# Performance work log

Hardware: AMD Instinct MI355X
Metric: run time of the kernel (lower is better)

## Reference

```python
import jax, jax.numpy as jnp
import numpy as np

DIM = 1024
HEADS = 16
HEAD_DIM = DIM // HEADS
EPS = 1e-5


def layer_norm(x, w, b):
    # normalize over last dim (head_dim)
    mu = jnp.mean(x, axis=-1, keepdims=True)
    var = jnp.mean(jnp.square(x - mu), axis=-1, keepdims=True)
    return (x - mu) * jax.lax.rsqrt(var + EPS) * w + b


def setup_inputs() -> dict:
    key = jax.random.key(0)
    ks = jax.random.split(key, 8)
    B, N = 2, 2048
    x = jax.random.normal(ks[0], (B, N, DIM), dtype=jnp.float32)
    mask = jax.random.randint(ks[1], (B, 1, N, N), 0, 2) == 1  # True = masked out
    qkv_w = jax.random.normal(ks[2], (3 * DIM, DIM), dtype=jnp.float32) * (DIM ** -0.5)
    q_norm_w = jnp.ones((HEAD_DIM,), dtype=jnp.float32)
    q_norm_b = jnp.zeros((HEAD_DIM,), dtype=jnp.float32)
    k_norm_w = jnp.ones((HEAD_DIM,), dtype=jnp.float32)
    k_norm_b = jnp.zeros((HEAD_DIM,), dtype=jnp.float32)
    proj_w = jax.random.normal(ks[3], (DIM, DIM), dtype=jnp.float32) * (DIM ** -0.5)
    proj_b = jnp.zeros((DIM,), dtype=jnp.float32)
    return {"x": x, "mask": mask, "qkv_w": qkv_w,
            "q_norm_w": q_norm_w, "q_norm_b": q_norm_b,
            "k_norm_w": k_norm_w, "k_norm_b": k_norm_b,
            "proj_w": proj_w, "proj_b": proj_b}


def reference(x, mask, qkv_w, q_norm_w, q_norm_b, k_norm_w, k_norm_b, proj_w, proj_b):
    B, N, C = x.shape
    H, D = HEADS, HEAD_DIM
    scale = D ** -0.5
    # qkv projection (no bias), split into q,k,v of shape (B,H,N,D)
    qkv = (x @ qkv_w.T).reshape(B, N, 3, H, D).transpose(2, 0, 3, 1, 4)
    q, k, v = qkv[0], qkv[1], qkv[2]
    q = layer_norm(q, q_norm_w, q_norm_b)
    k = layer_norm(k, k_norm_w, k_norm_b)
    q = q * scale
    attn = jnp.einsum("bhnd,bhmd->bhnm", q, k)  # (B,H,N,N)
    attn = jnp.where(mask, -jnp.inf, attn)
    attn = jax.nn.softmax(attn, axis=-1)
    out = jnp.einsum("bhnm,bhmd->bhnd", attn, v)
    out = out.transpose(0, 2, 1, 3).reshape(B, N, C)
    return out @ proj_w.T + proj_b
```

## Files before the change

### kernel.cpp

```cpp
#include <hip/hip_runtime.h>
#include <hip/hip_bf16.h>
#include <math.h>

#define B_    2
#define N_    2048
#define DIM_  1024
#define H_    16
#define HD_   64
#define EPS_  1e-5f
#define SCALE_ 0.125f
#define LOG2E_ 1.4426950408889634f
#define MFIX_  14.0f

typedef __attribute__((ext_vector_type(8))) __bf16 bf16x8;
typedef __attribute__((ext_vector_type(8))) unsigned short ushort8;
typedef __attribute__((ext_vector_type(4))) float f32x4;
typedef __attribute__((ext_vector_type(4))) unsigned int uint4v;

__device__ __forceinline__ unsigned short f2bf(float x) {
    unsigned u = __builtin_bit_cast(unsigned, x);
    u += 0x7fff + ((u >> 16) & 1);
    return (unsigned short)(u >> 16);
}
__device__ __forceinline__ unsigned pk2bf(float a, float b) {
    unsigned ua = __builtin_bit_cast(unsigned, a) + 0x8000u;
    unsigned ub = __builtin_bit_cast(unsigned, b) + 0x8000u;
    return __builtin_amdgcn_perm(ub, ua, 0x07060302);
}

__device__ __forceinline__ void gl_lds16(const void* g, void* l) {
    __builtin_amdgcn_global_load_lds(
        (const __attribute__((address_space(1))) void*)g,
        (__attribute__((address_space(3))) void*)l, 16, 0, 0);
}

__global__ __launch_bounds__(256) void cast_all_bf16(
    const float* __restrict__ x, const float* __restrict__ qkvw,
    const float* __restrict__ pw, unsigned short* __restrict__ out) {
    int i = (blockIdx.x * 256 + threadIdx.x) * 8;
    const float* src;
    if (i < 4194304) src = x + i;
    else if (i < 7340032) src = qkvw + (i - 4194304);
    else src = pw + (i - 7340032);
    float4 v0 = *(const float4*)src;
    float4 v1 = *(const float4*)(src + 4);
    ushort8 r;
    r[0] = f2bf(v0.x); r[1] = f2bf(v0.y); r[2] = f2bf(v0.z); r[3] = f2bf(v0.w);
    r[4] = f2bf(v1.x); r[5] = f2bf(v1.y); r[6] = f2bf(v1.z); r[7] = f2bf(v1.w);
    *(ushort8*)(out + i) = r;
}

__global__ __launch_bounds__(256) void pack_mask(
    const int* __restrict__ mask, unsigned long long* __restrict__ bm) {
    int w = blockIdx.x * 4 + (threadIdx.x >> 6);
    int lane = threadIdx.x & 63;
    int mv = mask[(size_t)w * 64 + lane];
    unsigned long long bits = __ballot(mv != 0);
    if (lane == 0) bm[w] = bits;
}

__global__ __launch_bounds__(256) void gemm_qkv_ln(
    const unsigned short* __restrict__ A, const unsigned short* __restrict__ Bw,
    const float* __restrict__ qnw, const float* __restrict__ qnb,
    const float* __restrict__ knw, const float* __restrict__ knb,
    unsigned short* __restrict__ qbuf, unsigned short* __restrict__ kbuf,
    unsigned short* __restrict__ vbuf) {
    const int K = DIM_;
    __shared__ unsigned short As[128 * 32];
    __shared__ unsigned short Bs[128 * 32];
    const int tid = threadIdx.x;
    const int wave = tid >> 6, lane = tid & 63;
    const int quad = lane >> 4, lcol = lane & 15;
    const int wr = wave >> 1, wc = wave & 1;
    const int row0 = blockIdx.y * 128, col0 = blockIdx.x * 128;

    f32x4 acc[4][4];
#pragma unroll
    for (int i = 0; i < 4; ++i)
#pragma unroll
        for (int j = 0; j < 4; ++j) acc[i][j] = (f32x4){0.f, 0.f, 0.f, 0.f};

    for (int k0 = 0; k0 < K; k0 += 32) {
        __syncthreads();
#pragma unroll
        for (int c = 0; c < 2; ++c) {
            int base = wave * 2048 + c * 1024;
            int myofs = base + lane * 16;
            int r = myofs >> 6;
            int kb = myofs & 63;
            gl_lds16((const char*)A + ((size_t)(row0 + r) * K + k0) * 2 + kb,
                     (char*)As + base);
            gl_lds16((const char*)Bw + ((size_t)(col0 + r) * K + k0) * 2 + kb,
                     (char*)Bs + base);
        }
        __syncthreads();

        bf16x8 af[4], bfr[4];
#pragma unroll
        for (int i = 0; i < 4; ++i) {
            af[i] = *(const bf16x8*)&As[(wr * 64 + i * 16 + lcol) * 32 + quad * 8];
            bfr[i] = *(const bf16x8*)&Bs[(wc * 64 + i * 16 + lcol) * 32 + quad * 8];
        }
#pragma unroll
        for (int i = 0; i < 4; ++i)
#pragma unroll
            for (int j = 0; j < 4; ++j)
                acc[i][j] = __builtin_amdgcn_mfma_f32_16x16x32_bf16(
                    af[i], bfr[j], acc[i][j], 0, 0, 0);
    }

    const int colbase = col0 + wc * 64;
    const int t = colbase >> 10;
    const int h = (colbase & 1023) >> 6;

    if (t < 2) {
        const float* wv = (t == 0) ? qnw : knw;
        const float* bv = (t == 0) ? qnb : knb;
        float wreg[4], breg[4];
#pragma unroll
        for (int j = 0; j < 4; ++j) {
            wreg[j] = wv[j * 16 + lcol];
            breg[j] = bv[j * 16 + lcol];
        }
        const float sc = (t == 0) ? (SCALE_ * LOG2E_) : 1.f;
        unsigned short* obase = (t == 0) ? qbuf : kbuf;
#pragma unroll
        for (int i = 0; i < 4; ++i) {
#pragma unroll
            for (int reg = 0; reg < 4; ++reg) {
                int row = row0 + wr * 64 + i * 16 + quad * 4 + reg;
                int bb = row >> 11, n = row & (N_ - 1);
                float v[4];
#pragma unroll
                for (int j = 0; j < 4; ++j) v[j] = acc[i][j][reg];
                float s = v[0] + v[1] + v[2] + v[3];
                s += __shfl_xor(s, 1);
                s += __shfl_xor(s, 2);
                s += __shfl_xor(s, 4);
                s += __shfl_xor(s, 8);
                float mu = s * (1.f / 64.f);
                float d[4], s2 = 0.f;
#pragma unroll
                for (int j = 0; j < 4; ++j) {
                    d[j] = v[j] - mu;
                    s2 += d[j] * d[j];
                }
                s2 += __shfl_xor(s2, 1);
                s2 += __shfl_xor(s2, 2);
                s2 += __shfl_xor(s2, 4);
                s2 += __shfl_xor(s2, 8);
                float r = rsqrtf(s2 * (1.f / 64.f) + EPS_);
                float o0 = (d[0] * r * wreg[0] + breg[0]) * sc;
                float o1 = (d[1] * r * wreg[1] + breg[1]) * sc;
                float o2 = (d[2] * r * wreg[2] + breg[2]) * sc;
                float o3 = (d[3] * r * wreg[3] + breg[3]) * sc;
                uint2 pk;
                pk.x = pk2bf(o0, o1);
                pk.y = pk2bf(o2, o3);
                *(uint2*)(obase + ((size_t)(bb * H_ + h) * N_ + n) * 64 +
                          lcol * 4) = pk;
            }
        }
    } else {
#pragma unroll
        for (int i = 0; i < 4; ++i) {
#pragma unroll
            for (int reg = 0; reg < 4; ++reg) {
                int row = row0 + wr * 64 + i * 16 + quad * 4 + reg;
                uint2 pk;
                pk.x = pk2bf(acc[i][0][reg], acc[i][1][reg]);
                pk.y = pk2bf(acc[i][2][reg], acc[i][3][reg]);
                *(uint2*)(vbuf + (size_t)row * DIM_ + h * 64 + lcol * 4) = pk;
            }
        }
    }
}

__global__ __launch_bounds__(256) void gemm_proj(
    const unsigned short* __restrict__ A, const unsigned short* __restrict__ Bw,
    const float* __restrict__ bias, float* __restrict__ Cout) {
    const int K = DIM_;
    __shared__ unsigned short As[128 * 32];
    __shared__ unsigned short Bs[64 * 32];
    const int tid = threadIdx.x;
    const int wave = tid >> 6, lane = tid & 63;
    const int quad = lane >> 4, lcol = lane & 15;
    const int row0 = blockIdx.y * 128, col0 = blockIdx.x * 64;

    f32x4 acc[2][4];
#pragma unroll
    for (int i = 0; i < 2; ++i)
#pragma unroll
        for (int j = 0; j < 4; ++j) acc[i][j] = (f32x4){0.f, 0.f, 0.f, 0.f};

    for (int k0 = 0; k0 < K; k0 += 32) {
        __syncthreads();
#pragma unroll
        for (int pi = 0; pi < 3; ++pi) {
            int p = wave * 3 + pi;
            if (p < 8) {
                int base = p * 1024;
                int myofs = base + lane * 16;
                int r = myofs >> 6, kb = myofs & 63;
                gl_lds16((const char*)A + ((size_t)(row0 + r) * K + k0) * 2 + kb,
                         (char*)As + base);
            } else {
                int base = (p - 8) * 1024;
                int myofs = base + lane * 16;
                int r = myofs >> 6, kb = myofs & 63;
                gl_lds16((const char*)Bw + ((size_t)(col0 + r) * K + k0) * 2 + kb,
                         (char*)Bs + base);
            }
        }
        __syncthreads();

        bf16x8 af[2], bfr[4];
#pragma unroll
        for (int i = 0; i < 2; ++i)
            af[i] = *(const bf16x8*)&As[(wave * 32 + i * 16 + lcol) * 32 + quad * 8];
#pragma unroll
        for (int j = 0; j < 4; ++j)
            bfr[j] = *(const bf16x8*)&Bs[(j * 16 + lcol) * 32 + quad * 8];
#pragma unroll
        for (int i = 0; i < 2; ++i)
#pragma unroll
            for (int j = 0; j < 4; ++j)
                acc[i][j] = __builtin_amdgcn_mfma_f32_16x16x32_bf16(
                    af[i], bfr[j], acc[i][j], 0, 0, 0);
    }

#pragma unroll
    for (int i = 0; i < 2; ++i) {
#pragma unroll
        for (int j = 0; j < 4; ++j) {
            int col = col0 + j * 16 + lcol;
            float bv = bias[col];
#pragma unroll
            for (int reg = 0; reg < 4; ++reg) {
                int row = row0 + wave * 32 + i * 16 + quad * 4 + reg;
                Cout[(size_t)row * DIM_ + col] = acc[i][j][reg] + bv;
            }
        }
    }
}

__global__ __launch_bounds__(256) void transpose_v(
    const unsigned short* __restrict__ vbuf, unsigned short* __restrict__ vt) {
    __shared__ unsigned short Ts[64 * 65];
    const int tid = threadIdx.x;
    const int bh = blockIdx.y, n0 = blockIdx.x * 64;
    const int b = bh >> 4, h = bh & 15;
    {
        int r = tid >> 2, s = tid & 3;
        const unsigned short* src =
            vbuf + (size_t)(b * N_ + n0 + r) * DIM_ + h * 64 + s * 16;
#pragma unroll
        for (int i = 0; i < 16; ++i) {
            int p = s * 16 + i;
            int trued = (p >> 2) + (p & 3) * 16;
            Ts[r * 65 + trued] = src[i];
        }
    }
    __syncthreads();
    {
        int d = tid >> 2, kt = tid & 3;
        unsigned short* dstrow = vt + (size_t)(bh * 64 + d) * N_ + n0;
        int P = kt >> 1, t = kt & 1;
#pragma unroll
        for (int q = 0; q < 4; ++q) {
            __align__(8) unsigned short tmp4[4];
#pragma unroll
            for (int j = 0; j < 4; ++j)
                tmp4[j] = Ts[(kt * 16 + q * 4 + j) * 65 + d];
            *(uint2*)(dstrow + P * 32 + q * 8 + t * 4) = *(const uint2*)tmp4;
        }
    }
}

__global__ __launch_bounds__(256, 2) void flash_attn_mfma7(
    const unsigned short* __restrict__ q, const unsigned short* __restrict__ k,
    const unsigned short* __restrict__ vt,
    const unsigned long long* __restrict__ bm, unsigned short* __restrict__ ao) {
    __shared__ unsigned short Qs[128 * 64];
    __shared__ unsigned short Ks[2][64 * 64];
    __shared__ unsigned short Vts[2][64 * 64];

    const int tid = threadIdx.x;
    const int wave = tid >> 6, lane = tid & 63;
    const int quad = lane >> 4, lcol = lane & 15;
    const int bh = blockIdx.y, b = bh >> 4, h = bh & 15;
    const int q0 = blockIdx.x * 128;

    const char* kgbase = (const char*)k + (size_t)bh * N_ * 128;
    const char* vtbase = (const char*)vt + (size_t)bh * 64 * N_ * 2;

    const char* kp[2];
    const char* vp[2];
#pragma unroll
    for (int ci = 0; ci < 2; ++ci) {
        int c = wave * 2 + ci;
        int swz = (c & 3) * 2;
        kp[ci] = kgbase + (size_t)(lane ^ swz) * 128 + c * 16;
        vp[ci] = vtbase + (size_t)(lane ^ swz) * N_ * 2 + c * 16;
    }

    {
        const char* qg = (const char*)(q + (size_t)(bh * N_ + q0) * 64);
#pragma unroll
        for (int c = 0; c < 4; ++c) {
            int base = wave * 4096 + c * 1024;
            gl_lds16(qg + base + lane * 16, (char*)Qs + base);
        }
#pragma unroll
        for (int ci = 0; ci < 2; ++ci) {
            int c = wave * 2 + ci;
            gl_lds16(kp[ci], (char*)Ks[0] + c * 1024);
            gl_lds16(vp[ci], (char*)Vts[0] + c * 1024);
            kp[ci] += 64 * 128;
            vp[ci] += 64 * 2;
        }
    }
    const unsigned long long* bmq0 =
        bm + ((size_t)b * N_ + q0 + wave * 32 + lcol) * 32;
    const unsigned long long* bmq1 = bmq0 + 16 * 32;
    unsigned long long mw_next0 = bmq0[0];
    unsigned long long mw_next1 = bmq1[0];
    __syncthreads();

    bf16x8 bq[2][2];
#pragma unroll
    for (int qf = 0; qf < 2; ++qf)
#pragma unroll
        for (int d0 = 0; d0 < 2; ++d0)
            bq[qf][d0] = *(const bf16x8*)&Qs[(wave * 32 + qf * 16 + lcol) * 64 +
                                             d0 * 32 + quad * 8];

    ushort8 ot;
#pragma unroll
    for (int i = 0; i < 8; ++i) ot[i] = 0x3F80;
    const bf16x8 ones = __builtin_bit_cast(bf16x8, ot);

    f32x4 oacc[2][4];
#pragma unroll
    for (int qf = 0; qf < 2; ++qf)
#pragma unroll
        for (int dt = 0; dt < 4; ++dt) oacc[qf][dt] = (f32x4){0.f, 0.f, 0.f, 0.f};
    f32x4 lacc[2];
    lacc[0] = (f32x4){0.f, 0.f, 0.f, 0.f};
    lacc[1] = (f32x4){0.f, 0.f, 0.f, 0.f};

    for (int k0 = 0; k0 < N_; k0 += 64) {
        const int cur = (k0 >> 6) & 1;
        const unsigned long long mw0 = mw_next0;
        const unsigned long long mw1 = mw_next1;
        if (k0 + 64 < N_) {
#pragma unroll
            for (int ci = 0; ci < 2; ++ci) {
                int c = wave * 2 + ci;
                gl_lds16(kp[ci], (char*)Ks[cur ^ 1] + c * 1024);
                gl_lds16(vp[ci], (char*)Vts[cur ^ 1] + c * 1024);
                kp[ci] += 64 * 128;
                vp[ci] += 64 * 2;
            }
            mw_next0 = bmq0[(k0 >> 6) + 1];
            mw_next1 = bmq1[(k0 >> 6) + 1];
        }

        f32x4 sacc[2][4];
#pragma unroll
        for (int qf = 0; qf < 2; ++qf) {
            unsigned long long mq = ((qf == 0) ? mw0 : mw1) >> (quad * 4);
            unsigned mlo = (unsigned)mq, mhi = (unsigned)(mq >> 32);
#pragma unroll
            for (int kt = 0; kt < 4; ++kt) {
                unsigned word = (kt < 2) ? mlo : mhi;
                const int sh = (kt & 1) * 16;
#pragma unroll
                for (int reg = 0; reg < 4; ++reg)
                    sacc[qf][kt][reg] =
                        ((word >> (sh + reg)) & 1u) ? -1e4f : -MFIX_;
            }
        }

        const char* ksb = (const char*)Ks[cur];
        const char* vsb = (const char*)Vts[cur];
#pragma unroll
        for (int kt = 0; kt < 4; ++kt) {
#pragma unroll
            for (int d0 = 0; d0 < 2; ++d0) {
                int p = d0 * 4 + quad;
                bf16x8 ak = *(const bf16x8*)(ksb + p * 1024 +
                                             (((kt * 16 + lcol) ^ (quad * 2)) << 4));
                sacc[0][kt] = __builtin_amdgcn_mfma_f32_16x16x32_bf16(
                    ak, bq[0][d0], sacc[0][kt], 0, 0, 0);
                sacc[1][kt] = __builtin_amdgcn_mfma_f32_16x16x32_bf16(
                    ak, bq[1][d0], sacc[1][kt], 0, 0, 0);
            }
        }

        uint2 pk[2][4];
#pragma unroll
        for (int qf = 0; qf < 2; ++qf) {
#pragma unroll
            for (int kt = 0; kt < 4; ++kt) {
                float p0 = exp2f(sacc[qf][kt][0]);
                float p1 = exp2f(sacc[qf][kt][1]);
                float p2 = exp2f(sacc[qf][kt][2]);
                float p3 = exp2f(sacc[qf][kt][3]);
                pk[qf][kt].x = pk2bf(p0, p1);
                pk[qf][kt].y = pk2bf(p2, p3);
            }
        }

#pragma unroll
        for (int P = 0; P < 2; ++P) {
            bf16x8 bp[2];
#pragma unroll
            for (int qf = 0; qf < 2; ++qf) {
                uint4v bu;
                bu[0] = pk[qf][2 * P].x;
                bu[1] = pk[qf][2 * P].y;
                bu[2] = pk[qf][2 * P + 1].x;
                bu[3] = pk[qf][2 * P + 1].y;
                bp[qf] = __builtin_bit_cast(bf16x8, bu);
                lacc[qf] = __builtin_amdgcn_mfma_f32_16x16x32_bf16(
                    ones, bp[qf], lacc[qf], 0, 0, 0);
            }
#pragma unroll
            for (int dt = 0; dt < 4; ++dt) {
                int c = P * 4 + quad;
                bf16x8 va = *(const bf16x8*)(vsb + c * 1024 +
                                             (((dt * 16 + lcol) ^ (quad * 2)) << 4));
                oacc[0][dt] = __builtin_amdgcn_mfma_f32_16x16x32_bf16(
                    va, bp[0], oacc[0][dt], 0, 0, 0);
                oacc[1][dt] = __builtin_amdgcn_mfma_f32_16x16x32_bf16(
                    va, bp[1], oacc[1][dt], 0, 0, 0);
            }
        }
        __syncthreads();
    }

#pragma unroll
    for (int qf = 0; qf < 2; ++qf) {
        float inv = 1.f / lacc[qf][0];
        int row = q0 + wave * 32 + qf * 16 + lcol;
        unsigned short* dst =
            ao + ((size_t)(b * N_ + row)) * DIM_ + h * 64 + quad * 4;
#pragma unroll
        for (int dt = 0; dt < 4; ++dt) {
            uint2 pko;
            pko.x = pk2bf(oacc[qf][dt][0] * inv, oacc[qf][dt][1] * inv);
            pko.y = pk2bf(oacc[qf][dt][2] * inv, oacc[qf][dt][3] * inv);
            *(uint2*)(dst + dt * 16) = pko;
        }
    }
}

extern "C" void kernel_launch(void* const* d_in, const int* in_sizes, int n_in,
                              void* d_out, int out_size, void* d_ws,
                              size_t ws_size, hipStream_t stream) {
    const float* x     = (const float*)d_in[0];
    const int*   mask  = (const int*)d_in[1];
    const float* qkv_w = (const float*)d_in[2];
    const float* qnw   = (const float*)d_in[3];
    const float* qnb   = (const float*)d_in[4];
    const float* knw   = (const float*)d_in[5];
    const float* knb   = (const float*)d_in[6];
    const float* pw    = (const float*)d_in[7];
    const float* pb    = (const float*)d_in[8];
    float* out = (float*)d_out;

    char* ws = (char*)d_ws;
    unsigned short* x_bf  = (unsigned short*)(ws + 0);
    unsigned short* qw_bf = (unsigned short*)(ws + 8388608);
    unsigned short* pw_bf = (unsigned short*)(ws + 14680064);
    unsigned short* qbuf  = (unsigned short*)(ws + 16777216);
    unsigned short* kbuf  = (unsigned short*)(ws + 25165824);
    unsigned short* vbuf  = (unsigned short*)(ws + 33554432);
    unsigned short* vt    = (unsigned short*)(ws + 41943040);
    unsigned long long* bmask = (unsigned long long*)(ws + 50331648);
    unsigned short* ao_bnc = vbuf;

    cast_all_bf16<<<8388608 / 2048, 256, 0, stream>>>(x, qkv_w, pw, x_bf);

    gemm_qkv_ln<<<dim3(3072 / 128, 4096 / 128), 256, 0, stream>>>(
        x_bf, qw_bf, qnw, qnb, knw, knb, qbuf, kbuf, vbuf);

    transpose_v<<<dim3(N_ / 64, B_ * H_), 256, 0, stream>>>(vbuf, vt);

    pack_mask<<<(B_ * N_ * (N_ / 64)) / 4, 256, 0, stream>>>(mask, bmask);

    flash_attn_mfma7<<<dim3(N_ / 128, B_ * H_), 256, 0, stream>>>(
        qbuf, kbuf, vt, bmask, ao_bnc);

    gemm_proj<<<dim3(DIM_ / 64, 4096 / 128), 256, 0, stream>>>(
        ao_bnc, pw_bf, pb, out);
}
```

Before: 278.3 us.

## Deepen flash-attention K/V prefetch to a 4-stage ring with explicit vmcnt waits

Replaces the double-buffered K/V LDS pipeline in the attention kernel with a 4-slot ring that keeps three tiles in flight, fully unrolled in groups of four. Each step waits with a hand-set s_waitcnt vmcnt count plus a barrier instead of __syncthreads, and the mask words are prefetched into per-slot registers. The aim is to hide global-to-LDS latency better. In exchange, LDS use doubles for K/V, which may limit occupancy, and the hard-coded vmcnt counts are fragile if the compiler emits a different number of memory ops.

```diff
diff --git a/kernel.cpp b/kernel.cpp
--- a/kernel.cpp
+++ b/kernel.cpp
@@ -277,13 +277,111 @@
     }
 }
 
-__global__ __launch_bounds__(256, 2) void flash_attn_mfma7(
+#define WAITBAR(Ncnt)                                                     \
+    asm volatile("s_waitcnt vmcnt(" #Ncnt ")" ::: "memory");              \
+    __builtin_amdgcn_s_barrier();                                         \
+    __builtin_amdgcn_sched_barrier(0);
+
+#define ISSUE(NF, PS)                                                     \
+    {                                                                     \
+        const int nf_ = (NF);                                             \
+        gl_lds16(kgbase + ((size_t)nf_ << 13) + klo0,                     \
+                 (char*)Ks[PS] + kld0);                                   \
+        gl_lds16(kgbase + ((size_t)nf_ << 13) + klo1,                     \
+                 (char*)Ks[PS] + kld1);                                   \
+        gl_lds16(vtbase + (size_t)nf_ * 128 + vlo0,                       \
+                 (char*)Vts[PS] + kld0);                                  \
+        gl_lds16(vtbase + (size_t)nf_ * 128 + vlo1,                       \
+                 (char*)Vts[PS] + kld1);                                  \
+        mm0[PS] = bmq0[nf_];                                              \
+        mm1[PS] = bmq1[nf_];                                              \
+    }
+
+#define COMPUTE(J)                                                        \
+    {                                                                     \
+        const unsigned long long mwa = mm0[J], mwb = mm1[J];              \
+        const char* ksb = (const char*)Ks[J];                             \
+        const char* vsb = (const char*)Vts[J];                            \
+        f32x4 sacc[2][4];                                                 \
+        {                                                                 \
+            unsigned long long mqa = mwa >> (quad * 4);                   \
+            unsigned long long mqb = mwb >> (quad * 4);                   \
+            unsigned ml[2][2];                                            \
+            ml[0][0] = (unsigned)mqa; ml[0][1] = (unsigned)(mqa >> 32);   \
+            ml[1][0] = (unsigned)mqb; ml[1][1] = (unsigned)(mqb >> 32);   \
+            _Pragma("unroll")                                             \
+            for (int qf = 0; qf < 2; ++qf) {                              \
+                _Pragma("unroll")                                         \
+                for (int kt = 0; kt < 4; ++kt) {                          \
+                    unsigned word = ml[qf][kt >> 1];                      \
+                    const int sh = (kt & 1) * 16;                         \
+                    _Pragma("unroll")                                     \
+                    for (int reg = 0; reg < 4; ++reg)                     \
+                        sacc[qf][kt][reg] =                               \
+                            ((word >> (sh + reg)) & 1u) ? -1e4f : -MFIX_; \
+                }                                                         \
+            }                                                             \
+        }                                                                 \
+        _Pragma("unroll")                                                 \
+        for (int kt = 0; kt < 4; ++kt) {                                  \
+            _Pragma("unroll")                                             \
+            for (int d0 = 0; d0 < 2; ++d0) {                              \
+                int p = d0 * 4 + quad;                                    \
+                bf16x8 ak = *(const bf16x8*)(ksb + p * 1024 +             \
+                    (((kt * 16 + lcol) ^ (quad * 2)) << 4));              \
+                sacc[0][kt] = __builtin_amdgcn_mfma_f32_16x16x32_bf16(    \
+                    ak, bq[0][d0], sacc[0][kt], 0, 0, 0);                 \
+                sacc[1][kt] = __builtin_amdgcn_mfma_f32_16x16x32_bf16(    \
+                    ak, bq[1][d0], sacc[1][kt], 0, 0, 0);                 \
+            }                                                             \
+        }                                                                 \
+        uint2 pk[2][4];                                                   \
+        _Pragma("unroll")                                                 \
+        for (int qf = 0; qf < 2; ++qf) {                                  \
+            _Pragma("unroll")                                             \
+            for (int kt = 0; kt < 4; ++kt) {                              \
+                float p0 = exp2f(sacc[qf][kt][0]);                        \
+                float p1 = exp2f(sacc[qf][kt][1]);                        \
+                float p2 = exp2f(sacc[qf][kt][2]);                        \
+                float p3 = exp2f(sacc[qf][kt][3]);                        \
+                pk[qf][kt].x = pk2bf(p0, p1);                             \
+                pk[qf][kt].y = pk2bf(p2, p3);                             \
+            }                                                             \
+        }                                                                 \
+        _Pragma("unroll")                                                 \
+        for (int P = 0; P < 2; ++P) {                                     \
+            bf16x8 bp[2];                                                 \
+            _Pragma("unroll")                                             \
+            for (int qf = 0; qf < 2; ++qf) {                              \
+                uint4v bu;                                                \
+                bu[0] = pk[qf][2 * P].x;                                  \
+                bu[1] = pk[qf][2 * P].y;                                  \
+                bu[2] = pk[qf][2 * P + 1].x;                              \
+                bu[3] = pk[qf][2 * P + 1].y;                              \
+                bp[qf] = __builtin_bit_cast(bf16x8, bu);                  \
+                lacc[qf] = __builtin_amdgcn_mfma_f32_16x16x32_bf16(       \
+                    ones, bp[qf], lacc[qf], 0, 0, 0);                     \
+            }                                                             \
+            _Pragma("unroll")                                             \
+            for (int dt = 0; dt < 4; ++dt) {                              \
+                int c = P * 4 + quad;                                     \
+                bf16x8 va = *(const bf16x8*)(vsb + c * 1024 +             \
+                    (((dt * 16 + lcol) ^ (quad * 2)) << 4));              \
+                oacc[0][dt] = __builtin_amdgcn_mfma_f32_16x16x32_bf16(    \
+                    va, bp[0], oacc[0][dt], 0, 0, 0);                     \
+                oacc[1][dt] = __builtin_amdgcn_mfma_f32_16x16x32_bf16(    \
+                    va, bp[1], oacc[1][dt], 0, 0, 0);                     \
+            }                                                             \
+        }                                                                 \
+    }
+
+__global__ __launch_bounds__(256, 2) void flash_attn_mfma8(
     const unsigned short* __restrict__ q, const unsigned short* __restrict__ k,
     const unsigned short* __restrict__ vt,
     const unsigned long long* __restrict__ bm, unsigned short* __restrict__ ao) {
     __shared__ unsigned short Qs[128 * 64];
-    __shared__ unsigned short Ks[2][64 * 64];
-    __shared__ unsigned short Vts[2][64 * 64];
+    __shared__ unsigned short Ks[4][64 * 64];
+    __shared__ unsigned short Vts[4][64 * 64];
 
     const int tid = threadIdx.x;
     const int wave = tid >> 6, lane = tid & 63;
@@ -294,15 +392,19 @@
     const char* kgbase = (const char*)k + (size_t)bh * N_ * 128;
     const char* vtbase = (const char*)vt + (size_t)bh * 64 * N_ * 2;
 
-    const char* kp[2];
-    const char* vp[2];
-#pragma unroll
-    for (int ci = 0; ci < 2; ++ci) {
-        int c = wave * 2 + ci;
-        int swz = (c & 3) * 2;
-        kp[ci] = kgbase + (size_t)(lane ^ swz) * 128 + c * 16;
-        vp[ci] = vtbase + (size_t)(lane ^ swz) * N_ * 2 + c * 16;
-    }
+    const int c0 = wave * 2, c1 = wave * 2 + 1;
+    const int swz0 = (c0 & 3) * 2, swz1 = (c1 & 3) * 2;
+    const int klo0 = (lane ^ swz0) * 128 + c0 * 16;
+    const int klo1 = (lane ^ swz1) * 128 + c1 * 16;
+    const size_t vlo0 = (size_t)(lane ^ swz0) * (N_ * 2) + c0 * 16;
+    const size_t vlo1 = (size_t)(lane ^ swz1) * (N_ * 2) + c1 * 16;
+    const int kld0 = c0 * 1024, kld1 = c1 * 1024;
+
+    const unsigned long long* bmq0 =
+        bm + ((size_t)b * N_ + q0 + wave * 32 + lcol) * 32;
+    const unsigned long long* bmq1 = bmq0 + 16 * 32;
+
+    unsigned long long mm0[4], mm1[4];
 
     {
         const char* qg = (const char*)(q + (size_t)(bh * N_ + q0) * 64);
@@ -311,21 +413,20 @@
             int base = wave * 4096 + c * 1024;
             gl_lds16(qg + base + lane * 16, (char*)Qs + base);
         }
-#pragma unroll
-        for (int ci = 0; ci < 2; ++ci) {
-            int c = wave * 2 + ci;
-            gl_lds16(kp[ci], (char*)Ks[0] + c * 1024);
-            gl_lds16(vp[ci], (char*)Vts[0] + c * 1024);
-            kp[ci] += 64 * 128;
-            vp[ci] += 64 * 2;
-        }
-    }
-    const unsigned long long* bmq0 =
-        bm + ((size_t)b * N_ + q0 + wave * 32 + lcol) * 32;
-    const unsigned long long* bmq1 = bmq0 + 16 * 32;
-    unsigned long long mw_next0 = bmq0[0];
-    unsigned long long mw_next1 = bmq1[0];
-    __syncthreads();
+    }
+    asm volatile("" ::: "memory");
+    __builtin_amdgcn_sched_barrier(0);
+#pragma unroll
+    for (int t = 0; t < 3; ++t) {
+        gl_lds16(kgbase + ((size_t)t << 13) + klo0, (char*)Ks[t] + kld0);
+        gl_lds16(kgbase + ((size_t)t << 13) + klo1, (char*)Ks[t] + kld1);
+        gl_lds16(vtbase + (size_t)t * 128 + vlo0, (char*)Vts[t] + kld0);
+        gl_lds16(vtbase + (size_t)t * 128 + vlo1, (char*)Vts[t] + kld1);
+        mm0[t] = bmq0[t];
+        mm1[t] = bmq1[t];
+    }
+    asm volatile("s_waitcnt vmcnt(18)" ::: "memory");
+    __builtin_amdgcn_sched_barrier(0);
 
     bf16x8 bq[2][2];
 #pragma unroll
@@ -349,96 +450,16 @@
     lacc[0] = (f32x4){0.f, 0.f, 0.f, 0.f};
     lacc[1] = (f32x4){0.f, 0.f, 0.f, 0.f};
 
-    for (int k0 = 0; k0 < N_; k0 += 64) {
-        const int cur = (k0 >> 6) & 1;
-        const unsigned long long mw0 = mw_next0;
-        const unsigned long long mw1 = mw_next1;
-        if (k0 + 64 < N_) {
-#pragma unroll
-            for (int ci = 0; ci < 2; ++ci) {
-                int c = wave * 2 + ci;
-                gl_lds16(kp[ci], (char*)Ks[cur ^ 1] + c * 1024);
-                gl_lds16(vp[ci], (char*)Vts[cur ^ 1] + c * 1024);
-                kp[ci] += 64 * 128;
-                vp[ci] += 64 * 2;
-            }
-            mw_next0 = bmq0[(k0 >> 6) + 1];
-            mw_next1 = bmq1[(k0 >> 6) + 1];
-        }
-
-        f32x4 sacc[2][4];
-#pragma unroll
-        for (int qf = 0; qf < 2; ++qf) {
-            unsigned long long mq = ((qf == 0) ? mw0 : mw1) >> (quad * 4);
-            unsigned mlo = (unsigned)mq, mhi = (unsigned)(mq >> 32);
-#pragma unroll
-            for (int kt = 0; kt < 4; ++kt) {
-                unsigned word = (kt < 2) ? mlo : mhi;
-                const int sh = (kt & 1) * 16;
-#pragma unroll
-                for (int reg = 0; reg < 4; ++reg)
-                    sacc[qf][kt][reg] =
-                        ((word >> (sh + reg)) & 1u) ? -1e4f : -MFIX_;
-            }
-        }
-
-        const char* ksb = (const char*)Ks[cur];
-        const char* vsb = (const char*)Vts[cur];
-#pragma unroll
-        for (int kt = 0; kt < 4; ++kt) {
-#pragma unroll
-            for (int d0 = 0; d0 < 2; ++d0) {
-                int p = d0 * 4 + quad;
-                bf16x8 ak = *(const bf16x8*)(ksb + p * 1024 +
-                                             (((kt * 16 + lcol) ^ (quad * 2)) << 4));
-                sacc[0][kt] = __builtin_amdgcn_mfma_f32_16x16x32_bf16(
-                    ak, bq[0][d0], sacc[0][kt], 0, 0, 0);
-                sacc[1][kt] = __builtin_amdgcn_mfma_f32_16x16x32_bf16(
-                    ak, bq[1][d0], sacc[1][kt], 0, 0, 0);
-            }
-        }
-
-        uint2 pk[2][4];
-#pragma unroll
-        for (int qf = 0; qf < 2; ++qf) {
-#pragma unroll
-            for (int kt = 0; kt < 4; ++kt) {
-                float p0 = exp2f(sacc[qf][kt][0]);
-                float p1 = exp2f(sacc[qf][kt][1]);
-                float p2 = exp2f(sacc[qf][kt][2]);
-                float p3 = exp2f(sacc[qf][kt][3]);
-                pk[qf][kt].x = pk2bf(p0, p1);
-                pk[qf][kt].y = pk2bf(p2, p3);
-            }
-        }
-
-#pragma unroll
-        for (int P = 0; P < 2; ++P) {
-            bf16x8 bp[2];
-#pragma unroll
-            for (int qf = 0; qf < 2; ++qf) {
-                uint4v bu;
-                bu[0] = pk[qf][2 * P].x;
-                bu[1] = pk[qf][2 * P].y;
-                bu[2] = pk[qf][2 * P + 1].x;
-                bu[3] = pk[qf][2 * P + 1].y;
-                bp[qf] = __builtin_bit_cast(bf16x8, bu);
-                lacc[qf] = __builtin_amdgcn_mfma_f32_16x16x32_bf16(
-                    ones, bp[qf], lacc[qf], 0, 0, 0);
-            }
-#pragma unroll
-            for (int dt = 0; dt < 4; ++dt) {
-                int c = P * 4 + quad;
-                bf16x8 va = *(const bf16x8*)(vsb + c * 1024 +
-                                             (((dt * 16 + lcol) ^ (quad * 2)) << 4));
-                oacc[0][dt] = __builtin_amdgcn_mfma_f32_16x16x32_bf16(
-                    va, bp[0], oacc[0][dt], 0, 0, 0);
-                oacc[1][dt] = __builtin_amdgcn_mfma_f32_16x16x32_bf16(
-                    va, bp[1], oacc[1][dt], 0, 0, 0);
-            }
-        }
-        __syncthreads();
-    }
+    for (int g = 0; g < 7; ++g) {
+        WAITBAR(12) ISSUE(g * 4 + 3, 3) COMPUTE(0)
+        WAITBAR(12) ISSUE(g * 4 + 4, 0) COMPUTE(1)
+        WAITBAR(12) ISSUE(g * 4 + 5, 1) COMPUTE(2)
+        WAITBAR(12) ISSUE(g * 4 + 6, 2) COMPUTE(3)
+    }
+    WAITBAR(12) ISSUE(31, 3) COMPUTE(0)
+    WAITBAR(12) COMPUTE(1)
+    WAITBAR(6)  COMPUTE(2)
+    WAITBAR(0)  COMPUTE(3)
 
 #pragma unroll
     for (int qf = 0; qf < 2; ++qf) {
@@ -490,7 +511,7 @@
 
     pack_mask<<<(B_ * N_ * (N_ / 64)) / 4, 256, 0, stream>>>(mask, bmask);
 
-    flash_attn_mfma7<<<dim3(N_ / 128, B_ * H_), 256, 0, stream>>>(
+    flash_attn_mfma8<<<dim3(N_ / 128, B_ * H_), 256, 0, stream>>>(
         qbuf, kbuf, vt, bmask, ao_bnc);
 
     gemm_proj<<<dim3(DIM_ / 64, 4096 / 128), 256, 0, stream>>>(
```

Result: no change. 276.0 us (-0.8%).
